# Performance work log

Hardware: AMD Instinct MI355X
Metric: run time of the kernel (lower is better)

Reference implementation:

```python
import jax, jax.numpy as jnp
import numpy as np

EPS = 1e-5
NUM_HEADS = 8
TOP_K = 2
CAP_FACTOR = 2  # capacity = CAP_FACTOR * T * TOP_K / E


def layernorm(x, g, b):
    m = jnp.mean(x, axis=-1, keepdims=True)
    v = jnp.var(x, axis=-1, keepdims=True)
    return (x - m) * jax.lax.rsqrt(v + EPS) * g + b


def setup_inputs() -> dict:
    key = jax.random.key(0)
    ks = jax.random.split(key, 16)
    B, S, H, E, F = 2, 2048, 512, 64, 2048
    s = 0.02
    return {
        "x": jax.random.normal(ks[0], (B, S, H), jnp.float32),
        "ln1_g": jnp.ones((H,), jnp.float32),
        "ln1_b": jnp.zeros((H,), jnp.float32),
        "wq": jax.random.normal(ks[1], (H, H), jnp.float32) * s,
        "wk": jax.random.normal(ks[2], (H, H), jnp.float32) * s,
        "wv": jax.random.normal(ks[3], (H, H), jnp.float32) * s,
        "wo": jax.random.normal(ks[4], (H, H), jnp.float32) * s,
        "ln2_g": jnp.ones((H,), jnp.float32),
        "ln2_b": jnp.zeros((H,), jnp.float32),
        "wr": jax.random.normal(ks[5], (H, E), jnp.float32) * s,
        "w1": jax.random.normal(ks[6], (E, H, F), jnp.float32) * s,
        "b1": jnp.zeros((E, F), jnp.float32),
        "w2": jax.random.normal(ks[7], (E, F, H), jnp.float32) * s,
        "b2": jnp.zeros((E, H), jnp.float32),
    }


def reference(x, ln1_g, ln1_b, wq, wk, wv, wo, ln2_g, ln2_b, wr, w1, b1, w2, b2):
    B, S, H = x.shape
    NH = NUM_HEADS
    dh = H // NH

    # ---- pre-norm multi-head self-attention + residual ----
    x1 = layernorm(x, ln1_g, ln1_b)
    q = (x1 @ wq).reshape(B, S, NH, dh)
    k = (x1 @ wk).reshape(B, S, NH, dh)
    v = (x1 @ wv).reshape(B, S, NH, dh)
    scores = jnp.einsum("bqhd,bkhd->bhqk", q, k) * (dh ** -0.5)
    p = jax.nn.softmax(scores, axis=-1)
    attn_out = jnp.einsum("bhqk,bkhd->bqhd", p, v).reshape(B, S, H) @ wo
    x = x + attn_out

    # ---- pre-norm top-2 MoE + residual ----
    x2 = layernorm(x, ln2_g, ln2_b).reshape(B * S, H)  # [T, H]
    T = B * S
    E = wr.shape[1]
    C = CAP_FACTOR * (T * TOP_K // E)  # expert capacity

    probs = jax.nn.softmax(x2 @ wr, axis=-1)            # [T, E]
    gate_v, gate_i = jax.lax.top_k(probs, TOP_K)        # [T, K]
    gate_v = gate_v / jnp.sum(gate_v, axis=-1, keepdims=True)

    ef = gate_i.reshape(-1)                              # [T*K] expert per slot
    gf = gate_v.reshape(-1)                              # [T*K] gate per slot
    oh = jax.nn.one_hot(ef, E, dtype=x2.dtype)           # [T*K, E]
    # position of each slot within its expert queue
    pos = jnp.sum((jnp.cumsum(oh, axis=0) - oh) * oh, axis=1).astype(jnp.int32)
    keep = (pos < C).astype(x2.dtype)                    # drop overflow tokens
    posc = jnp.minimum(pos, C - 1)

    tok = jnp.repeat(x2, TOP_K, axis=0) * keep[:, None]  # [T*K, H]
    buf = jnp.zeros((E, C, H), x2.dtype).at[ef, posc].add(tok)  # dispatch

    h = jax.nn.gelu(jnp.einsum("ech,ehf->ecf", buf, w1) + b1[:, None, :])
    y = jnp.einsum("ecf,efh->ech", h, w2) + b2[:, None, :]

    ys = y[ef, posc] * (gf * keep)[:, None]              # combine, [T*K, H]
    moe_out = ys.reshape(T, TOP_K, H).sum(axis=1).reshape(B, S, H)
    return x + moe_out
```

## Files before the change

kernel.cpp:

```cpp
#include <hip/hip_runtime.h>
#include <hip/hip_bf16.h>
#include <math.h>

constexpr int Bc  = 2;
constexpr int Sc  = 2048;
constexpr int Hc  = 512;
constexpr int NHc = 8;
constexpr int Tc  = Bc * Sc;
constexpr int Ec  = 64;
constexpr int Fc  = 2048;
constexpr int Cap = 256;

typedef __attribute__((ext_vector_type(8))) short bf16x8;
typedef __attribute__((ext_vector_type(4))) float f32x4;

__device__ __forceinline__ unsigned short f2b(float f) {
    union { float f; unsigned u; } v; v.f = f;
    unsigned r = v.u + 0x7FFF + ((v.u >> 16) & 1);
    return (unsigned short)(r >> 16);
}

__device__ __forceinline__ unsigned cvt_pk_bf16(float lo, float hi) {
    unsigned r;
    asm volatile("v_cvt_pk_bf16_f32 %0, %1, %2" : "=v"(r) : "v"(lo), "v"(hi));
    return r;
}

__device__ __forceinline__ float gelu_f(float x) {
    float x3 = x * x * x;
    return 0.5f * x * (1.0f + tanhf(0.7978845608028654f * (x + 0.044715f * x3)));
}

template <typename TO>
__global__ __launch_bounds__(256) void ln_kernel(const float* __restrict__ x,
                                                 const float* __restrict__ g,
                                                 const float* __restrict__ b,
                                                 TO* __restrict__ o) {
    int t = blockIdx.x;
    const float* row = x + (size_t)t * Hc;
    int tid = threadIdx.x;
    float v0 = row[tid];
    float v1 = row[tid + 256];
    float s = v0 + v1, s2 = v0 * v0 + v1 * v1;
    for (int off = 32; off; off >>= 1) {
        s  += __shfl_down(s,  off);
        s2 += __shfl_down(s2, off);
    }
    __shared__ float ls[4], ls2[4];
    int wid = tid >> 6, lane = tid & 63;
    if (lane == 0) { ls[wid] = s; ls2[wid] = s2; }
    __syncthreads();
    if (tid == 0) {
        float a = 0.f, a2 = 0.f;
        for (int i = 0; i < 4; i++) { a += ls[i]; a2 += ls2[i]; }
        ls[0] = a; ls2[0] = a2;
    }
    __syncthreads();
    float mean = ls[0] * (1.0f / Hc);
    float var  = ls2[0] * (1.0f / Hc) - mean * mean;
    float r = rsqrtf(var + 1e-5f);
    float o0 = (v0 - mean) * r * g[tid]       + b[tid];
    float o1 = (v1 - mean) * r * g[tid + 256] + b[tid + 256];
    if constexpr (sizeof(TO) == 2) {
        o[(size_t)t * Hc + tid]       = (TO)f2b(o0);
        o[(size_t)t * Hc + tid + 256] = (TO)f2b(o1);
    } else {
        o[(size_t)t * Hc + tid]       = o0;
        o[(size_t)t * Hc + tid + 256] = o1;
    }
}

template <int BM, int EPI, int SWZ, typename TC>
__global__ __launch_bounds__(BM * 2) void gemm_mfma(const unsigned short* __restrict__ A,
                                                    const float* __restrict__ W,
                                                    TC* __restrict__ C,
                                                    const float* __restrict__ X,
                                                    int M, int N, int K,
                                                    long sA, long sW, long sC, long sX,
                                                    const float* __restrict__ Wb,
                                                    const float* __restrict__ Wc) {
    int bx = blockIdx.x, bz = blockIdx.z, by = blockIdx.y;
    if (SWZ) {
        int gx = gridDim.x;
        int nwg = gx * gridDim.z;
        int flat = bx + gx * bz;
        int wg = (flat & 7) * (nwg >> 3) + (flat >> 3);
        bx = wg % gx; bz = wg / gx;
    }
    A += (size_t)bz * sA;
    if (Wb) W = (bz == 0) ? W : ((bz == 1) ? Wb : Wc);
    else    W += (size_t)bz * sW;
    C += (size_t)bz * sC;
    if (X) X += (size_t)bz * sX;
    int m0 = by * BM, n0 = bx * 128;

    __shared__ unsigned short As[BM * 72];
    __shared__ unsigned short Bs[128 * 72];

    int tid = threadIdx.x;
    int wid = tid >> 6, lane = tid & 63;
    int wr = (wid >> 1) * 64, wc = (wid & 1) * 64;
    int lr = lane & 15, lg = lane >> 4;

    f32x4 acc[4][4];
    #pragma unroll
    for (int i = 0; i < 4; i++)
        #pragma unroll
        for (int j = 0; j < 4; j++) acc[i][j] = (f32x4){0.f, 0.f, 0.f, 0.f};

    for (int k0 = 0; k0 < K; k0 += 64) {
        #pragma unroll
        for (int p = 0; p < 4; p++) {
            int e = p * 16 * BM + tid * 8;
            int row = e >> 6, col = e & 63;
            *(bf16x8*)&As[row * 72 + col] =
                *(const bf16x8*)&A[(size_t)(m0 + row) * K + k0 + col];
        }
        #pragma unroll
        for (int p = 0; p < 512 / BM; p++) {
            int kp = (tid >> 5) + p * (BM / 16);
            int c  = (tid & 31) * 4;
            const float* w0 = &W[(size_t)(k0 + 2 * kp) * N + n0 + c];
            float4 a = *(const float4*)w0;
            float4 b = *(const float4*)(w0 + N);
            int qz = 8 * ((c >> 3) & 7);
            int kof = (2 * kp) ^ qz;
            *(ushort2*)&Bs[(c + 0) * 72 + kof] = (ushort2){f2b(a.x), f2b(b.x)};
            *(ushort2*)&Bs[(c + 1) * 72 + kof] = (ushort2){f2b(a.y), f2b(b.y)};
            *(ushort2*)&Bs[(c + 2) * 72 + kof] = (ushort2){f2b(a.z), f2b(b.z)};
            *(ushort2*)&Bs[(c + 3) * 72 + kof] = (ushort2){f2b(a.w), f2b(b.w)};
        }
        __syncthreads();
        #pragma unroll
        for (int kk = 0; kk < 64; kk += 32) {
            bf16x8 af[4], bfr[4];
            #pragma unroll
            for (int i = 0; i < 4; i++) {
                af[i] = *(const bf16x8*)&As[(wr + i * 16 + lr) * 72 + kk + 8 * lg];
                int nrow = wc + i * 16 + lr;
                int qq = 8 * ((nrow >> 3) & 7);
                bfr[i] = *(const bf16x8*)&Bs[nrow * 72 + ((kk + 8 * lg) ^ qq)];
            }
            #pragma unroll
            for (int i = 0; i < 4; i++)
                #pragma unroll
                for (int j = 0; j < 4; j++)
                    acc[i][j] = __builtin_amdgcn_mfma_f32_16x16x32_bf16(af[i], bfr[j], acc[i][j], 0, 0, 0);
        }
        __syncthreads();
    }

    #pragma unroll
    for (int i = 0; i < 4; i++) {
        #pragma unroll
        for (int r = 0; r < 4; r++) {
            int m = m0 + wr + i * 16 + lg * 4 + r;
            #pragma unroll
            for (int j = 0; j < 4; j++) {
                int n = n0 + wc + j * 16 + lr;
                float vv = acc[i][j][r];
                if (EPI == 1) vv += X[(size_t)m * N + n];
                if (EPI == 2) { vv += X[n]; vv = gelu_f(vv); }
                if (EPI == 3) vv += X[n];
                if constexpr (sizeof(TC) == 2) C[(size_t)m * N + n] = (TC)f2b(vv);
                else                            C[(size_t)m * N + n] = vv;
            }
        }
    }
}

__global__ __launch_bounds__(256) void attn_mfma_kernel(const unsigned short* __restrict__ q,
                                                        const unsigned short* __restrict__ k,
                                                        const unsigned short* __restrict__ v,
                                                        unsigned short* __restrict__ o) {
    constexpr int LDK = 72;
    constexpr int NT  = Sc / 64;
    __shared__ unsigned short Ks[2][64 * LDK];
    __shared__ unsigned short Vt[2][64 * LDK];

    int flat = blockIdx.x;
    int wg = (flat & 7) * 64 + (flat >> 3);
    int qt = wg & 31;
    int hb = wg >> 5;
    int hh = hb & 7, b = hb >> 3;

    int q0 = qt * 64;
    int tid = threadIdx.x;
    int wid = tid >> 6, lane = tid & 63;
    int lr = lane & 15, lg = lane >> 4;

    const unsigned short* kbase = k + (size_t)(b * Sc) * Hc + hh * 64;
    const unsigned short* vbase = v + (size_t)(b * Sc) * Hc + hh * 64;

    bf16x8 qf[2];
    {
        const unsigned short* qrow = q + ((size_t)(b * Sc + q0 + wid * 16 + lr)) * Hc + hh * 64;
        qf[0] = *(const bf16x8*)&qrow[8 * lg];
        qf[1] = *(const bf16x8*)&qrow[32 + 8 * lg];
    }

    int krow = tid >> 3;
    int kcol = (tid & 7) * 8;
    int vk2  = (tid >> 4) * 2;
    int vd4  = (tid & 15) * 4;

    bf16x8 kr[2];
    ushort4 va[2], vb2[2];

    auto load_tile = [&](int kt) {
        #pragma unroll
        for (int p = 0; p < 2; p++) {
            kr[p] = *(const bf16x8*)&kbase[(size_t)(kt * 64 + p * 32 + krow) * Hc + kcol];
            const unsigned short* vp = &vbase[(size_t)(kt * 64 + p * 32 + vk2) * Hc + vd4];
            va[p]  = *(const ushort4*)vp;
            vb2[p] = *(const ushort4*)(vp + Hc);
        }
    };
    auto vswz = [](int d, int c) { return c ^ (8 * ((d >> 3) & 7)); };
    auto store_tile = [&](int bu) {
        #pragma unroll
        for (int p = 0; p < 2; p++) {
            *(bf16x8*)&Ks[bu][(p * 32 + krow) * LDK + kcol] = kr[p];
            int k2 = p * 32 + vk2;
            *(ushort2*)&Vt[bu][(vd4 + 0) * LDK + vswz(vd4 + 0, k2)] = (ushort2){va[p].x, vb2[p].x};
            *(ushort2*)&Vt[bu][(vd4 + 1) * LDK + vswz(vd4 + 1, k2)] = (ushort2){va[p].y, vb2[p].y};
            *(ushort2*)&Vt[bu][(vd4 + 2) * LDK + vswz(vd4 + 2, k2)] = (ushort2){va[p].z, vb2[p].z};
            *(ushort2*)&Vt[bu][(vd4 + 3) * LDK + vswz(vd4 + 3, k2)] = (ushort2){va[p].w, vb2[p].w};
        }
    };

    f32x4 Oacc[4];
    #pragma unroll
    for (int nb = 0; nb < 4; nb++) Oacc[nb] = (f32x4){0.f, 0.f, 0.f, 0.f};
    float mrun = -1e30f, lrun = 0.f;
    const float SCL2 = 0.125f * 1.4426950408889634f;

    load_tile(0);
    store_tile(0);
    __syncthreads();

    for (int kt = 0; kt < NT; kt++) {
        int cur = kt & 1;
        if (kt + 1 < NT) load_tile(kt + 1);

        f32x4 sacc[4];
        #pragma unroll
        for (int kb = 0; kb < 4; kb++) sacc[kb] = (f32x4){0.f, 0.f, 0.f, 0.f};
        __builtin_amdgcn_s_setprio(1);
        #pragma unroll
        for (int kb = 0; kb < 4; kb++) {
            #pragma unroll
            for (int s = 0; s < 2; s++) {
                bf16x8 kf = *(const bf16x8*)&Ks[cur][(kb * 16 + lr) * LDK + 32 * s + 8 * lg];
                sacc[kb] = __builtin_amdgcn_mfma_f32_16x16x32_bf16(kf, qf[s], sacc[kb], 0, 0, 0);
            }
        }
        __builtin_amdgcn_s_setprio(0);

        float z[4][4];
        float mt = -1e30f;
        #pragma unroll
        for (int kb = 0; kb < 4; kb++)
            #pragma unroll
            for (int r = 0; r < 4; r++) {
                z[kb][r] = sacc[kb][r] * SCL2;
                mt = fmaxf(mt, z[kb][r]);
            }
        mt = fmaxf(mt, __shfl_xor(mt, 16));
        mt = fmaxf(mt, __shfl_xor(mt, 32));

        bool defer = __all(mt - mrun <= 11.0f);
        float pv[4][4];
        float ps = 0.f;
        if (defer) {
            #pragma unroll
            for (int kb = 0; kb < 4; kb++)
                #pragma unroll
                for (int r = 0; r < 4; r++) {
                    pv[kb][r] = __builtin_amdgcn_exp2f(z[kb][r] - mrun);
                    ps += pv[kb][r];
                }
            ps += __shfl_xor(ps, 16);
            ps += __shfl_xor(ps, 32);
            lrun += ps;
        } else {
            float mnew = fmaxf(mrun, mt);
            float sc = __builtin_amdgcn_exp2f(mrun - mnew);
            #pragma unroll
            for (int kb = 0; kb < 4; kb++)
                #pragma unroll
                for (int r = 0; r < 4; r++) {
                    pv[kb][r] = __builtin_amdgcn_exp2f(z[kb][r] - mnew);
                    ps += pv[kb][r];
                }
            ps += __shfl_xor(ps, 16);
            ps += __shfl_xor(ps, 32);
            lrun = lrun * sc + ps;
            mrun = mnew;
            float scb[4];
            #pragma unroll
            for (int r = 0; r < 4; r++) scb[r] = __shfl(sc, lg * 4 + r);
            #pragma unroll
            for (int nb = 0; nb < 4; nb++)
                #pragma unroll
                for (int r = 0; r < 4; r++) Oacc[nb][r] *= scb[r];
        }

        unsigned d_[4][2];
        #pragma unroll
        for (int kb = 0; kb < 4; kb++) {
            d_[kb][0] = cvt_pk_bf16(pv[kb][0], pv[kb][1]);
            d_[kb][1] = cvt_pk_bf16(pv[kb][2], pv[kb][3]);
        }
        unsigned pfw[2][4];
        #pragma unroll
        for (int s = 0; s < 2; s++) {
            #pragma unroll
            for (int h = 0; h < 2; h++) {
                unsigned xx = d_[2 * s][h], yy = d_[2 * s + 1][h];
                asm volatile("v_permlane32_swap_b32 %0, %1" : "+v"(xx), "+v"(yy));
                asm volatile("v_permlane16_swap_b32 %0, %1" : "+v"(xx), "+v"(yy));
                pfw[s][h]     = xx;
                pfw[s][2 + h] = yy;
            }
        }
        bf16x8 pf0, pf1;
        *(unsigned*)&((short*)&pf0)[0] = pfw[0][0];
        *(unsigned*)&((short*)&pf0)[2] = pfw[0][1];
        *(unsigned*)&((short*)&pf0)[4] = pfw[0][2];
        *(unsigned*)&((short*)&pf0)[6] = pfw[0][3];
        *(unsigned*)&((short*)&pf1)[0] = pfw[1][0];
        *(unsigned*)&((short*)&pf1)[2] = pfw[1][1];
        *(unsigned*)&((short*)&pf1)[4] = pfw[1][2];
        *(unsigned*)&((short*)&pf1)[6] = pfw[1][3];

        __builtin_amdgcn_s_setprio(1);
        #pragma unroll
        for (int nb = 0; nb < 4; nb++) {
            f32x4 oa = Oacc[nb];
            int vrow = nb * 16 + lr;
            bf16x8 vf0 = *(const bf16x8*)&Vt[cur][vrow * LDK + vswz(vrow, 8 * lg)];
            bf16x8 vf1 = *(const bf16x8*)&Vt[cur][vrow * LDK + vswz(vrow, 32 + 8 * lg)];
            oa = __builtin_amdgcn_mfma_f32_16x16x32_bf16(pf0, vf0, oa, 0, 0, 0);
            oa = __builtin_amdgcn_mfma_f32_16x16x32_bf16(pf1, vf1, oa, 0, 0, 0);
            Oacc[nb] = oa;
        }
        __builtin_amdgcn_s_setprio(0);

        if (kt + 1 < NT) store_tile(cur ^ 1);
        __syncthreads();
    }

    float linv = 1.0f / lrun;
    unsigned short* ob = o + ((size_t)(b * Sc + q0 + wid * 16)) * Hc + hh * 64;
    #pragma unroll
    for (int r = 0; r < 4; r++) {
        float invB = __shfl(linv, lg * 4 + r);
        #pragma unroll
        for (int nb = 0; nb < 4; nb++) {
            ob[(size_t)(lg * 4 + r) * Hc + nb * 16 + lr] = f2b(Oacc[nb][r] * invB);
        }
    }
}

__global__ __launch_bounds__(256) void router_top2_kernel(const float* __restrict__ x2,
                                                          const float* __restrict__ wr,
                                                          int* __restrict__ ef,
                                                          float* __restrict__ gf) {
    int t = blockIdx.x * 4 + (threadIdx.x >> 6);
    int l = threadIdx.x & 63;
    const float* xr = x2 + (size_t)t * Hc;
    float acc = 0.f;
    for (int hhh = 0; hhh < Hc; hhh++) acc += xr[hhh] * wr[hhh * Ec + l];

    float mx = acc;
    for (int off = 32; off; off >>= 1) mx = fmaxf(mx, __shfl_xor(mx, off));
    float p = expf(acc - mx);
    float sum = p;
    for (int off = 32; off; off >>= 1) sum += __shfl_xor(sum, off);
    p /= sum;

    float v1 = p; int i1 = l;
    for (int off = 32; off; off >>= 1) {
        float ov = __shfl_xor(v1, off);
        int   oi = __shfl_xor(i1, off);
        if (ov > v1 || (ov == v1 && oi < i1)) { v1 = ov; i1 = oi; }
    }
    float v2 = (l == i1) ? -INFINITY : p; int i2 = l;
    for (int off = 32; off; off >>= 1) {
        float ov = __shfl_xor(v2, off);
        int   oi = __shfl_xor(i2, off);
        if (ov > v2 || (ov == v2 && oi < i2)) { v2 = ov; i2 = oi; }
    }
    if (l == 0) {
        float inv = 1.0f / (v1 + v2);
        ef[t * 2]     = i1;
        ef[t * 2 + 1] = i2;
        gf[t * 2]     = v1 * inv;
        gf[t * 2 + 1] = v2 * inv;
    }
}

__global__ __launch_bounds__(256) void pos_kernel(const int* __restrict__ ef,
                                                  int* __restrict__ pos) {
    int e = blockIdx.x;
    __shared__ int cnts[257];
    int tid = threadIdx.x;
    int base = tid * 32;
    int c = 0;
    for (int i = 0; i < 32; i++) c += (ef[base + i] == e) ? 1 : 0;
    cnts[tid + 1] = c;
    if (tid == 0) cnts[0] = 0;
    __syncthreads();
    if (tid == 0) {
        for (int i = 1; i <= 256; i++) cnts[i] += cnts[i - 1];
    }
    __syncthreads();
    int run = cnts[tid];
    for (int i = 0; i < 32; i++) {
        if (ef[base + i] == e) pos[base + i] = run++;
    }
}

__global__ __launch_bounds__(128) void dispatch_kernel(const float* __restrict__ x2,
                                                       const int* __restrict__ ef,
                                                       const int* __restrict__ pos,
                                                       unsigned short* __restrict__ buf) {
    int s = blockIdx.x;
    int p = pos[s];
    if (p >= Cap) return;
    int e = ef[s];
    int t = s >> 1;
    float4 vv = ((const float4*)(x2 + (size_t)t * Hc))[threadIdx.x];
    ushort4 o;
    o.x = f2b(vv.x); o.y = f2b(vv.y); o.z = f2b(vv.z); o.w = f2b(vv.w);
    ((ushort4*)(buf + ((size_t)e * Cap + p) * Hc))[threadIdx.x] = o;
}

__global__ __launch_bounds__(128) void combine_kernel(const float* __restrict__ xa,
                                                      const float* __restrict__ y,
                                                      const int* __restrict__ ef,
                                                      const int* __restrict__ pos,
                                                      const float* __restrict__ gf,
                                                      float* __restrict__ out) {
    int t = blockIdx.x;
    int d = threadIdx.x;
    float4 acc = ((const float4*)(xa + (size_t)t * Hc))[d];
    #pragma unroll
    for (int kk = 0; kk < 2; kk++) {
        int s = t * 2 + kk;
        int p = pos[s];
        if (p < Cap) {
            float w = gf[s];
            float4 yv = ((const float4*)(y + ((size_t)ef[s] * Cap + p) * Hc))[d];
            acc.x += w * yv.x;
            acc.y += w * yv.y;
            acc.z += w * yv.z;
            acc.w += w * yv.w;
        }
    }
    ((float4*)(out + (size_t)t * Hc))[d] = acc;
}

extern "C" void kernel_launch(void* const* d_in, const int* in_sizes, int n_in,
                              void* d_out, int out_size, void* d_ws, size_t ws_size,
                              hipStream_t stream) {
    const float* x     = (const float*)d_in[0];
    const float* ln1_g = (const float*)d_in[1];
    const float* ln1_b = (const float*)d_in[2];
    const float* wq    = (const float*)d_in[3];
    const float* wk    = (const float*)d_in[4];
    const float* wv    = (const float*)d_in[5];
    const float* wo    = (const float*)d_in[6];
    const float* ln2_g = (const float*)d_in[7];
    const float* ln2_b = (const float*)d_in[8];
    const float* wr    = (const float*)d_in[9];
    const float* w1    = (const float*)d_in[10];
    const float* b1    = (const float*)d_in[11];
    const float* w2    = (const float*)d_in[12];
    const float* b2    = (const float*)d_in[13];
    float* out = (float*)d_out;

    const size_t TH   = (size_t)Tc * Hc;
    const size_t ECH  = (size_t)Ec * Cap * Hc;
    const size_t ECF  = (size_t)Ec * Cap * Fc;
    const size_t HF   = (size_t)Hc * Fc;

    char* wsb = (char*)d_ws;
    size_t off = 0;
    auto alloc = [&](size_t bytes) { size_t r = off; off = (off + bytes + 255) & ~(size_t)255; return r; };
    size_t x1b_off = alloc(TH * 2);
    size_t qkv_off = alloc(TH * 2 * 3);
    size_t ab_off  = alloc(TH * 2);
    size_t xa_off  = alloc(TH * 4);
    size_t x2_off  = alloc(TH * 4);
    size_t ef_off  = alloc((size_t)Tc * 2 * 4);
    size_t pos_off = alloc((size_t)Tc * 2 * 4);
    size_t gf_off  = alloc((size_t)Tc * 2 * 4);
    size_t buf_off = alloc(ECH * 2);
    size_t h_off   = alloc(ECF * 2);
    size_t y_off   = alloc(ECH * 4);
    if (ws_size < off) return;

    unsigned short* x1b  = (unsigned short*)(wsb + x1b_off);
    unsigned short* qb   = (unsigned short*)(wsb + qkv_off);
    unsigned short* kb   = qb + TH;
    unsigned short* vb   = qb + 2 * TH;
    unsigned short* ab   = (unsigned short*)(wsb + ab_off);
    float* xa  = (float*)(wsb + xa_off);
    float* x2  = (float*)(wsb + x2_off);
    int*   ef  = (int*)(wsb + ef_off);
    int*   pos = (int*)(wsb + pos_off);
    float* gf  = (float*)(wsb + gf_off);
    unsigned short* bufb = (unsigned short*)(wsb + buf_off);
    unsigned short* h    = (unsigned short*)(wsb + h_off);
    float* y = (float*)(wsb + y_off);

    dim3 blk(256);

    ln_kernel<unsigned short><<<Tc, blk, 0, stream>>>(x, ln1_g, ln1_b, x1b);

    gemm_mfma<128, 0, 0, unsigned short><<<dim3(Hc / 128, Tc / 128, 3), blk, 0, stream>>>(
        x1b, wq, qb, nullptr, Tc, Hc, Hc, 0, 0, (long)TH, 0, wk, wv);

    attn_mfma_kernel<<<dim3(512), blk, 0, stream>>>(qb, kb, vb, ab);

    gemm_mfma<128, 1, 0, float><<<dim3(Hc / 128, Tc / 128, 1), blk, 0, stream>>>(
        ab, wo, xa, x, Tc, Hc, Hc, 0, 0, 0, 0, nullptr, nullptr);

    ln_kernel<float><<<Tc, blk, 0, stream>>>(xa, ln2_g, ln2_b, x2);

    router_top2_kernel<<<Tc / 4, blk, 0, stream>>>(x2, wr, ef, gf);

    pos_kernel<<<Ec, blk, 0, stream>>>(ef, pos);

    dispatch_kernel<<<Tc * 2, dim3(128), 0, stream>>>(x2, ef, pos, bufb);

    gemm_mfma<256, 2, 1, unsigned short><<<dim3(Fc / 128, Cap / 256, Ec), dim3(512), 0, stream>>>(
        bufb, w1, h, b1, Cap, Fc, Hc,
        (long)Cap * Hc, (long)HF, (long)Cap * Fc, (long)Fc, nullptr, nullptr);

    gemm_mfma<256, 3, 1, float><<<dim3(Hc / 128, Cap / 256, Ec), dim3(512), 0, stream>>>(
        h, w2, y, b2, Cap, Hc, Fc,
        (long)Cap * Fc, (long)HF, (long)Cap * Hc, (long)Hc, nullptr, nullptr);

    combine_kernel<<<Tc, dim3(128), 0, stream>>>(xa, y, ef, pos, gf, out);
}
```

Measured before the change: 348.3 us.

## Prefetch GEMM tiles into registers, fuse LN2 with router, shrink intermediates to bf16

Result: faster. 291.6 us (median of 2 runs) (-16.3%).

```diff
diff --git a/kernel.cpp b/kernel.cpp
--- a/kernel.cpp
+++ b/kernel.cpp
@@ -20,6 +20,10 @@
     return (unsigned short)(r >> 16);
 }
 
+__device__ __forceinline__ float b2f(unsigned short u) {
+    union { unsigned u; float f; } v; v.u = ((unsigned)u) << 16; return v.f;
+}
+
 __device__ __forceinline__ unsigned cvt_pk_bf16(float lo, float hi) {
     unsigned r;
     asm volatile("v_cvt_pk_bf16_f32 %0, %1, %2" : "=v"(r) : "v"(lo), "v"(hi));
@@ -27,47 +31,43 @@
 }
 
 __device__ __forceinline__ float gelu_f(float x) {
-    float x3 = x * x * x;
-    return 0.5f * x * (1.0f + tanhf(0.7978845608028654f * (x + 0.044715f * x3)));
-}
-
-template <typename TO>
-__global__ __launch_bounds__(256) void ln_kernel(const float* __restrict__ x,
-                                                 const float* __restrict__ g,
-                                                 const float* __restrict__ b,
-                                                 TO* __restrict__ o) {
-    int t = blockIdx.x;
-    const float* row = x + (size_t)t * Hc;
-    int tid = threadIdx.x;
-    float v0 = row[tid];
-    float v1 = row[tid + 256];
-    float s = v0 + v1, s2 = v0 * v0 + v1 * v1;
+    float u = x + 0.044715f * x * x * x;
+    float r = __builtin_amdgcn_exp2f(-2.302211692851f * u);
+    return x * __builtin_amdgcn_rcpf(1.0f + r);
+}
+
+__global__ __launch_bounds__(256) void ln_rows_kernel(const float* __restrict__ x,
+                                                      const float* __restrict__ g,
+                                                      const float* __restrict__ b,
+                                                      unsigned short* __restrict__ o) {
+    int w = threadIdx.x >> 6, l = threadIdx.x & 63;
+    int t = blockIdx.x * 4 + w;
+    const float4* row = (const float4*)(x + (size_t)t * Hc);
+    float4 a = row[l], c = row[l + 64];
+    float s  = a.x + a.y + a.z + a.w + c.x + c.y + c.z + c.w;
+    float s2 = a.x * a.x + a.y * a.y + a.z * a.z + a.w * a.w
+             + c.x * c.x + c.y * c.y + c.z * c.z + c.w * c.w;
+    #pragma unroll
     for (int off = 32; off; off >>= 1) {
-        s  += __shfl_down(s,  off);
-        s2 += __shfl_down(s2, off);
-    }
-    __shared__ float ls[4], ls2[4];
-    int wid = tid >> 6, lane = tid & 63;
-    if (lane == 0) { ls[wid] = s; ls2[wid] = s2; }
-    __syncthreads();
-    if (tid == 0) {
-        float a = 0.f, a2 = 0.f;
-        for (int i = 0; i < 4; i++) { a += ls[i]; a2 += ls2[i]; }
-        ls[0] = a; ls2[0] = a2;
-    }
-    __syncthreads();
-    float mean = ls[0] * (1.0f / Hc);
-    float var  = ls2[0] * (1.0f / Hc) - mean * mean;
+        s  += __shfl_xor(s,  off);
+        s2 += __shfl_xor(s2, off);
+    }
+    float mean = s * (1.0f / Hc);
+    float var  = s2 * (1.0f / Hc) - mean * mean;
     float r = rsqrtf(var + 1e-5f);
-    float o0 = (v0 - mean) * r * g[tid]       + b[tid];
-    float o1 = (v1 - mean) * r * g[tid + 256] + b[tid + 256];
-    if constexpr (sizeof(TO) == 2) {
-        o[(size_t)t * Hc + tid]       = (TO)f2b(o0);
-        o[(size_t)t * Hc + tid + 256] = (TO)f2b(o1);
-    } else {
-        o[(size_t)t * Hc + tid]       = o0;
-        o[(size_t)t * Hc + tid + 256] = o1;
-    }
+    float4 g0 = ((const float4*)g)[l], g1 = ((const float4*)g)[l + 64];
+    float4 b0 = ((const float4*)b)[l], b1 = ((const float4*)b)[l + 64];
+    ushort4 u0, u1;
+    u0.x = f2b((a.x - mean) * r * g0.x + b0.x);
+    u0.y = f2b((a.y - mean) * r * g0.y + b0.y);
+    u0.z = f2b((a.z - mean) * r * g0.z + b0.z);
+    u0.w = f2b((a.w - mean) * r * g0.w + b0.w);
+    u1.x = f2b((c.x - mean) * r * g1.x + b1.x);
+    u1.y = f2b((c.y - mean) * r * g1.y + b1.y);
+    u1.z = f2b((c.z - mean) * r * g1.z + b1.z);
+    u1.w = f2b((c.w - mean) * r * g1.w + b1.w);
+    ((ushort4*)(o + (size_t)t * Hc))[l]      = u0;
+    ((ushort4*)(o + (size_t)t * Hc))[l + 64] = u1;
 }
 
 template <int BM, int EPI, int SWZ, typename TC>
@@ -102,35 +102,59 @@
     int wr = (wid >> 1) * 64, wc = (wid & 1) * 64;
     int lr = lane & 15, lg = lane >> 4;
 
+    constexpr int WP = 512 / BM;
+    bf16x8 areg[4];
+    float4 wa[WP], wb[WP];
+
+    auto load_tile = [&](int k0) {
+        #pragma unroll
+        for (int p = 0; p < 4; p++) {
+            int e = p * 16 * BM + tid * 8;
+            int row = e >> 6, col = e & 63;
+            areg[p] = *(const bf16x8*)&A[(size_t)(m0 + row) * K + k0 + col];
+        }
+        #pragma unroll
+        for (int p = 0; p < WP; p++) {
+            int kp = (tid >> 5) + p * (BM / 16);
+            int c  = (tid & 31) * 4;
+            const float* w0 = &W[(size_t)(k0 + 2 * kp) * N + n0 + c];
+            wa[p] = *(const float4*)w0;
+            wb[p] = *(const float4*)(w0 + N);
+        }
+    };
+    auto write_tile = [&]() {
+        #pragma unroll
+        for (int p = 0; p < 4; p++) {
+            int e = p * 16 * BM + tid * 8;
+            int row = e >> 6, col = e & 63;
+            *(bf16x8*)&As[row * 72 + col] = areg[p];
+        }
+        #pragma unroll
+        for (int p = 0; p < WP; p++) {
+            int kp = (tid >> 5) + p * (BM / 16);
+            int c  = (tid & 31) * 4;
+            int qz = 8 * ((c >> 3) & 7);
+            int kof = (2 * kp) ^ qz;
+            *(ushort2*)&Bs[(c + 0) * 72 + kof] = (ushort2){f2b(wa[p].x), f2b(wb[p].x)};
+            *(ushort2*)&Bs[(c + 1) * 72 + kof] = (ushort2){f2b(wa[p].y), f2b(wb[p].y)};
+            *(ushort2*)&Bs[(c + 2) * 72 + kof] = (ushort2){f2b(wa[p].z), f2b(wb[p].z)};
+            *(ushort2*)&Bs[(c + 3) * 72 + kof] = (ushort2){f2b(wa[p].w), f2b(wb[p].w)};
+        }
+    };
+
     f32x4 acc[4][4];
     #pragma unroll
     for (int i = 0; i < 4; i++)
         #pragma unroll
         for (int j = 0; j < 4; j++) acc[i][j] = (f32x4){0.f, 0.f, 0.f, 0.f};
 
-    for (int k0 = 0; k0 < K; k0 += 64) {
-        #pragma unroll
-        for (int p = 0; p < 4; p++) {
-            int e = p * 16 * BM + tid * 8;
-            int row = e >> 6, col = e & 63;
-            *(bf16x8*)&As[row * 72 + col] =
-                *(const bf16x8*)&A[(size_t)(m0 + row) * K + k0 + col];
-        }
-        #pragma unroll
-        for (int p = 0; p < 512 / BM; p++) {
-            int kp = (tid >> 5) + p * (BM / 16);
-            int c  = (tid & 31) * 4;
-            const float* w0 = &W[(size_t)(k0 + 2 * kp) * N + n0 + c];
-            float4 a = *(const float4*)w0;
-            float4 b = *(const float4*)(w0 + N);
-            int qz = 8 * ((c >> 3) & 7);
-            int kof = (2 * kp) ^ qz;
-            *(ushort2*)&Bs[(c + 0) * 72 + kof] = (ushort2){f2b(a.x), f2b(b.x)};
-            *(ushort2*)&Bs[(c + 1) * 72 + kof] = (ushort2){f2b(a.y), f2b(b.y)};
-            *(ushort2*)&Bs[(c + 2) * 72 + kof] = (ushort2){f2b(a.z), f2b(b.z)};
-            *(ushort2*)&Bs[(c + 3) * 72 + kof] = (ushort2){f2b(a.w), f2b(b.w)};
-        }
-        __syncthreads();
+    load_tile(0);
+    int nsteps = K >> 6;
+    for (int s = 0; s < nsteps; s++) {
+        write_tile();
+        if (s + 1 < nsteps) load_tile((s + 1) << 6);
+        asm volatile("s_waitcnt lgkmcnt(0)" ::: "memory");
+        __builtin_amdgcn_s_barrier();
         #pragma unroll
         for (int kk = 0; kk < 64; kk += 32) {
             bf16x8 af[4], bfr[4];
@@ -147,7 +171,8 @@
                 for (int j = 0; j < 4; j++)
                     acc[i][j] = __builtin_amdgcn_mfma_f32_16x16x32_bf16(af[i], bfr[j], acc[i][j], 0, 0, 0);
         }
-        __syncthreads();
+        asm volatile("s_waitcnt lgkmcnt(0)" ::: "memory");
+        __builtin_amdgcn_s_barrier();
     }
 
     #pragma unroll
@@ -363,41 +388,79 @@
     }
 }
 
-__global__ __launch_bounds__(256) void router_top2_kernel(const float* __restrict__ x2,
-                                                          const float* __restrict__ wr,
-                                                          int* __restrict__ ef,
-                                                          float* __restrict__ gf) {
-    int t = blockIdx.x * 4 + (threadIdx.x >> 6);
-    int l = threadIdx.x & 63;
-    const float* xr = x2 + (size_t)t * Hc;
+__global__ __launch_bounds__(256) void ln2_router_kernel(const float* __restrict__ xa,
+                                                         const float* __restrict__ g,
+                                                         const float* __restrict__ b,
+                                                         const float* __restrict__ wr,
+                                                         unsigned short* __restrict__ x2b,
+                                                         int* __restrict__ ef,
+                                                         float* __restrict__ gf) {
+    int t = blockIdx.x;
+    const float* row = xa + (size_t)t * Hc;
+    int tid = threadIdx.x;
+    int w = tid >> 6, l = tid & 63;
+    float v0 = row[tid];
+    float v1 = row[tid + 256];
+    float s = v0 + v1, s2 = v0 * v0 + v1 * v1;
+    for (int off = 32; off; off >>= 1) {
+        s  += __shfl_down(s,  off);
+        s2 += __shfl_down(s2, off);
+    }
+    __shared__ float ls[4], ls2[4];
+    __shared__ float xn[512];
+    __shared__ float part[4][64];
+    if (l == 0) { ls[w] = s; ls2[w] = s2; }
+    __syncthreads();
+    if (tid == 0) {
+        float a = 0.f, a2 = 0.f;
+        for (int i = 0; i < 4; i++) { a += ls[i]; a2 += ls2[i]; }
+        ls[0] = a; ls2[0] = a2;
+    }
+    __syncthreads();
+    float mean = ls[0] * (1.0f / Hc);
+    float var  = ls2[0] * (1.0f / Hc) - mean * mean;
+    float r = rsqrtf(var + 1e-5f);
+    float o0 = (v0 - mean) * r * g[tid]       + b[tid];
+    float o1 = (v1 - mean) * r * g[tid + 256] + b[tid + 256];
+    xn[tid] = o0; xn[tid + 256] = o1;
+    x2b[(size_t)t * Hc + tid]       = f2b(o0);
+    x2b[(size_t)t * Hc + tid + 256] = f2b(o1);
+    __syncthreads();
+
     float acc = 0.f;
-    for (int hhh = 0; hhh < Hc; hhh++) acc += xr[hhh] * wr[hhh * Ec + l];
-
-    float mx = acc;
-    for (int off = 32; off; off >>= 1) mx = fmaxf(mx, __shfl_xor(mx, off));
-    float p = expf(acc - mx);
-    float sum = p;
-    for (int off = 32; off; off >>= 1) sum += __shfl_xor(sum, off);
-    p /= sum;
-
-    float v1 = p; int i1 = l;
-    for (int off = 32; off; off >>= 1) {
-        float ov = __shfl_xor(v1, off);
-        int   oi = __shfl_xor(i1, off);
-        if (ov > v1 || (ov == v1 && oi < i1)) { v1 = ov; i1 = oi; }
-    }
-    float v2 = (l == i1) ? -INFINITY : p; int i2 = l;
-    for (int off = 32; off; off >>= 1) {
-        float ov = __shfl_xor(v2, off);
-        int   oi = __shfl_xor(i2, off);
-        if (ov > v2 || (ov == v2 && oi < i2)) { v2 = ov; i2 = oi; }
-    }
-    if (l == 0) {
-        float inv = 1.0f / (v1 + v2);
-        ef[t * 2]     = i1;
-        ef[t * 2 + 1] = i2;
-        gf[t * 2]     = v1 * inv;
-        gf[t * 2 + 1] = v2 * inv;
+    const float* wrow = wr + (size_t)(w * 128) * Ec + l;
+    #pragma unroll 8
+    for (int hh = 0; hh < 128; hh++)
+        acc += xn[w * 128 + hh] * wrow[(size_t)hh * Ec];
+    part[w][l] = acc;
+    __syncthreads();
+    if (w == 0) {
+        float logit = part[0][l] + part[1][l] + part[2][l] + part[3][l];
+        float mx = logit;
+        for (int off = 32; off; off >>= 1) mx = fmaxf(mx, __shfl_xor(mx, off));
+        float p = __expf(logit - mx);
+        float sum = p;
+        for (int off = 32; off; off >>= 1) sum += __shfl_xor(sum, off);
+        p /= sum;
+        float v1_ = p; int i1 = l;
+        for (int off = 32; off; off >>= 1) {
+            float ov = __shfl_xor(v1_, off);
+            int   oi = __shfl_xor(i1, off);
+            if (ov > v1_ || (ov == v1_ && oi < i1)) { v1_ = ov; i1 = oi; }
+        }
+        float v2_ = (l == i1) ? -INFINITY : p; int i2 = l;
+        for (int off = 32; off; off >>= 1) {
+            float ov = __shfl_xor(v2_, off);
+            int   oi = __shfl_xor(i2, off);
+            if (ov > v2_ || (ov == v2_ && oi < i2)) { v2_ = ov; i2 = oi; }
+        }
+        if (l == 0) {
+            float inv = 1.0f / (v1_ + v2_);
+            ef[t * 2]     = i1;
+            ef[t * 2 + 1] = i2;
+            gf[t * 2]     = v1_ * inv;
+            gf[t * 2 + 1] = v2_ * inv;
+        }
     }
 }
 
@@ -412,17 +475,21 @@
     cnts[tid + 1] = c;
     if (tid == 0) cnts[0] = 0;
     __syncthreads();
-    if (tid == 0) {
-        for (int i = 1; i <= 256; i++) cnts[i] += cnts[i - 1];
-    }
-    __syncthreads();
+    #pragma unroll
+    for (int off = 1; off < 256; off <<= 1) {
+        int v = cnts[tid + 1];
+        int add = (tid + 1 > off) ? cnts[tid + 1 - off] : 0;
+        __syncthreads();
+        cnts[tid + 1] = v + add;
+        __syncthreads();
+    }
     int run = cnts[tid];
     for (int i = 0; i < 32; i++) {
         if (ef[base + i] == e) pos[base + i] = run++;
     }
 }
 
-__global__ __launch_bounds__(128) void dispatch_kernel(const float* __restrict__ x2,
+__global__ __launch_bounds__(128) void dispatch_kernel(const unsigned short* __restrict__ x2b,
                                                        const int* __restrict__ ef,
                                                        const int* __restrict__ pos,
                                                        unsigned short* __restrict__ buf) {
@@ -431,14 +498,12 @@
     if (p >= Cap) return;
     int e = ef[s];
     int t = s >> 1;
-    float4 vv = ((const float4*)(x2 + (size_t)t * Hc))[threadIdx.x];
-    ushort4 o;
-    o.x = f2b(vv.x); o.y = f2b(vv.y); o.z = f2b(vv.z); o.w = f2b(vv.w);
-    ((ushort4*)(buf + ((size_t)e * Cap + p) * Hc))[threadIdx.x] = o;
+    ushort4 vv = ((const ushort4*)(x2b + (size_t)t * Hc))[threadIdx.x];
+    ((ushort4*)(buf + ((size_t)e * Cap + p) * Hc))[threadIdx.x] = vv;
 }
 
 __global__ __launch_bounds__(128) void combine_kernel(const float* __restrict__ xa,
-                                                      const float* __restrict__ y,
+                                                      const unsigned short* __restrict__ y,
                                                       const int* __restrict__ ef,
                                                       const int* __restrict__ pos,
                                                       const float* __restrict__ gf,
@@ -452,11 +517,11 @@
         int p = pos[s];
         if (p < Cap) {
             float w = gf[s];
-            float4 yv = ((const float4*)(y + ((size_t)ef[s] * Cap + p) * Hc))[d];
-            acc.x += w * yv.x;
-            acc.y += w * yv.y;
-            acc.z += w * yv.z;
-            acc.w += w * yv.w;
+            ushort4 yv = ((const ushort4*)(y + ((size_t)ef[s] * Cap + p) * Hc))[d];
+            acc.x += w * b2f(yv.x);
+            acc.y += w * b2f(yv.y);
+            acc.z += w * b2f(yv.z);
+            acc.w += w * b2f(yv.w);
         }
     }
     ((float4*)(out + (size_t)t * Hc))[d] = acc;
@@ -493,13 +558,13 @@
     size_t qkv_off = alloc(TH * 2 * 3);
     size_t ab_off  = alloc(TH * 2);
     size_t xa_off  = alloc(TH * 4);
-    size_t x2_off  = alloc(TH * 4);
+    size_t x2b_off = alloc(TH * 2);
     size_t ef_off  = alloc((size_t)Tc * 2 * 4);
     size_t pos_off = alloc((size_t)Tc * 2 * 4);
     size_t gf_off  = alloc((size_t)Tc * 2 * 4);
     size_t buf_off = alloc(ECH * 2);
     size_t h_off   = alloc(ECF * 2);
-    size_t y_off   = alloc(ECH * 4);
+    size_t y_off   = alloc(ECH * 2);
     if (ws_size < off) return;
 
     unsigned short* x1b  = (unsigned short*)(wsb + x1b_off);
@@ -508,17 +573,17 @@
     unsigned short* vb   = qb + 2 * TH;
     unsigned short* ab   = (unsigned short*)(wsb + ab_off);
     float* xa  = (float*)(wsb + xa_off);
-    float* x2  = (float*)(wsb + x2_off);
+    unsigned short* x2b = (unsigned short*)(wsb + x2b_off);
     int*   ef  = (int*)(wsb + ef_off);
     int*   pos = (int*)(wsb + pos_off);
     float* gf  = (float*)(wsb + gf_off);
     unsigned short* bufb = (unsigned short*)(wsb + buf_off);
     unsigned short* h    = (unsigned short*)(wsb + h_off);
-    float* y = (float*)(wsb + y_off);
+    unsigned short* y    = (unsigned short*)(wsb + y_off);
 
     dim3 blk(256);
 
-    ln_kernel<unsigned short><<<Tc, blk, 0, stream>>>(x, ln1_g, ln1_b, x1b);
+    ln_rows_kernel<<<Tc / 4, blk, 0, stream>>>(x, ln1_g, ln1_b, x1b);
 
     gemm_mfma<128, 0, 0, unsigned short><<<dim3(Hc / 128, Tc / 128, 3), blk, 0, stream>>>(
         x1b, wq, qb, nullptr, Tc, Hc, Hc, 0, 0, (long)TH, 0, wk, wv);
@@ -528,19 +593,17 @@
     gemm_mfma<128, 1, 0, float><<<dim3(Hc / 128, Tc / 128, 1), blk, 0, stream>>>(
         ab, wo, xa, x, Tc, Hc, Hc, 0, 0, 0, 0, nullptr, nullptr);
 
-    ln_kernel<float><<<Tc, blk, 0, stream>>>(xa, ln2_g, ln2_b, x2);
-
-    router_top2_kernel<<<Tc / 4, blk, 0, stream>>>(x2, wr, ef, gf);
+    ln2_router_kernel<<<Tc, blk, 0, stream>>>(xa, ln2_g, ln2_b, wr, x2b, ef, gf);
 
     pos_kernel<<<Ec, blk, 0, stream>>>(ef, pos);
 
-    dispatch_kernel<<<Tc * 2, dim3(128), 0, stream>>>(x2, ef, pos, bufb);
+    dispatch_kernel<<<Tc * 2, dim3(128), 0, stream>>>(x2b, ef, pos, bufb);
 
     gemm_mfma<256, 2, 1, unsigned short><<<dim3(Fc / 128, Cap / 256, Ec), dim3(512), 0, stream>>>(
         bufb, w1, h, b1, Cap, Fc, Hc,
         (long)Cap * Hc, (long)HF, (long)Cap * Fc, (long)Fc, nullptr, nullptr);
 
-    gemm_mfma<256, 3, 1, float><<<dim3(Hc / 128, Cap / 256, Ec), dim3(512), 0, stream>>>(
+    gemm_mfma<256, 3, 1, unsigned short><<<dim3(Hc / 128, Cap / 256, Ec), dim3(512), 0, stream>>>(
         h, w2, y, b2, Cap, Hc, Fc,
         (long)Cap * Fc, (long)HF, (long)Cap * Hc, (long)Hc, nullptr, nullptr);
 
```
